# Optimization experiments

Measured on AMD Instinct MI355X. Metric: run time of the kernel, lower is better.

Reference implementation:

```python
import jax, jax.numpy as jnp
import numpy as np

B, T, C = 2, 1024, 2048
E, TOPK = 8, 2
F_MOE = 1408
F_SHARED = 5632


def setup_inputs() -> dict:
    key = jax.random.key(0)
    ks = jax.random.split(key, 9)
    s = 0.02
    return {
        "x": jax.random.normal(ks[0], (B, T, C), dtype=jnp.float32),
        "gate_w": jax.random.normal(ks[1], (E, C), dtype=jnp.float32) * s,
        "expert_fc1": jax.random.normal(ks[2], (E, F_MOE, C), dtype=jnp.float32) * s,
        "expert_fc2": jax.random.normal(ks[3], (E, F_MOE, C), dtype=jnp.float32) * s,
        "expert_proj": jax.random.normal(ks[4], (E, C, F_MOE), dtype=jnp.float32) * s,
        "shared_fc1": jax.random.normal(ks[5], (F_SHARED, C), dtype=jnp.float32) * s,
        "shared_fc2": jax.random.normal(ks[6], (F_SHARED, C), dtype=jnp.float32) * s,
        "shared_proj": jax.random.normal(ks[7], (C, F_SHARED), dtype=jnp.float32) * s,
        "shared_gate_w": jax.random.normal(ks[8], (1, C), dtype=jnp.float32) * s,
    }


def reference(x, gate_w, expert_fc1, expert_fc2, expert_proj,
              shared_fc1, shared_fc2, shared_proj, shared_gate_w):
    b, t, c = x.shape
    xf = x.reshape(-1, c)                                   # [N, C]
    n = xf.shape[0]

    # router: softmax in fp32, then top-k
    router = xf @ gate_w.T                                  # [N, E]
    probs = jax.nn.softmax(router.astype(jnp.float32), axis=1).astype(x.dtype)
    top_p, top_i = jax.lax.top_k(probs, TOPK)               # [N, k]

    # dense combine weights: prob where selected else 0 (top-k indices are distinct)
    combine = jnp.zeros((n, E), dtype=x.dtype).at[
        jnp.arange(n)[:, None], top_i].set(top_p)            # [N, E]

    # per-expert SwiGLU MLP, computed densely then weighted by combine
    h1 = jnp.einsum('nc,efc->enf', xf, expert_fc1)          # [E, N, F]
    h2 = jnp.einsum('nc,efc->enf', xf, expert_fc2)
    h = jax.nn.silu(h1) * h2
    out_e = jnp.einsum('enf,ecf->enc', h, expert_proj)      # [E, N, C]
    y = jnp.einsum('ne,enc->nc', combine, out_e)            # [N, C]

    # shared expert with sigmoid gate
    s1 = xf @ shared_fc1.T
    s2 = xf @ shared_fc2.T
    shared = (jax.nn.silu(s1) * s2) @ shared_proj.T         # [N, C]
    y = y + jax.nn.sigmoid(xf @ shared_gate_w.T) * shared
    return y.reshape(b, t, c)
```

## Files before the change

kernel.cpp:

```cpp
#include <hip/hip_runtime.h>
#include <hip/hip_bf16.h>
#include <math.h>
#include <stdint.h>

#define N_TOK   2048
#define C_DIM   2048
#define E_NUM   8
#define F_MOE   1408
#define F_SH    5632
#define SLOTS   4096
#define PADROWS 4608

typedef __bf16 bf16;
typedef __bf16 bf16x8 __attribute__((ext_vector_type(8)));
typedef __bf16 bf16x4 __attribute__((ext_vector_type(4)));
typedef float  f32x4  __attribute__((ext_vector_type(4)));

__device__ __forceinline__ f32x4 mfma16(bf16x8 a, bf16x8 b, f32x4 c) {
    return __builtin_amdgcn_mfma_f32_16x16x32_bf16(a, b, c, 0, 0, 0);
}
__device__ __forceinline__ void gload16(const void* g, void* l) {
    __builtin_amdgcn_global_load_lds(
        (const __attribute__((address_space(1))) void*)g,
        (__attribute__((address_space(3))) void*)l, 16, 0, 0);
}
#define RAWBAR()  asm volatile("s_barrier" ::: "memory")
#define VMCNT12() asm volatile("s_waitcnt vmcnt(12)" ::: "memory")
#define VMCNT8()  asm volatile("s_waitcnt vmcnt(8)" ::: "memory")
#define VMCNT4()  asm volatile("s_waitcnt vmcnt(4)" ::: "memory")
#define VMCNT0()  asm volatile("s_waitcnt vmcnt(0)" ::: "memory")

__global__ void router_kernel(const float* __restrict__ x,
                              const float* __restrict__ gate_w,
                              const float* __restrict__ sgate_w,
                              int* __restrict__ slotexp,
                              float* __restrict__ slotp,
                              float* __restrict__ sig)
{
    const int n   = blockIdx.x;
    const int tid = threadIdx.x;
    const float* xr = x + (size_t)n * C_DIM;
    const int c0 = tid * 8;

    float xv[8];
#pragma unroll
    for (int j = 0; j < 8; ++j) xv[j] = xr[c0 + j];

    float dots[9];
#pragma unroll
    for (int e = 0; e < 9; ++e) {
        const float* wr = (e < 8) ? (gate_w + (size_t)e * C_DIM) : sgate_w;
        float p = 0.f;
#pragma unroll
        for (int j = 0; j < 8; ++j) p += xv[j] * wr[c0 + j];
#pragma unroll
        for (int off = 32; off > 0; off >>= 1) p += __shfl_down(p, off);
        dots[e] = p;
    }

    __shared__ float red[4][9];
    const int wid = tid >> 6, lane = tid & 63;
    if (lane == 0) {
#pragma unroll
        for (int e = 0; e < 9; ++e) red[wid][e] = dots[e];
    }
    __syncthreads();
    if (tid == 0) {
        float l[9];
#pragma unroll
        for (int e = 0; e < 9; ++e)
            l[e] = red[0][e] + red[1][e] + red[2][e] + red[3][e];
        float mx = l[0];
#pragma unroll
        for (int e = 1; e < 8; ++e) mx = fmaxf(mx, l[e]);
        float p[8], s = 0.f;
#pragma unroll
        for (int e = 0; e < 8; ++e) { p[e] = expf(l[e] - mx); s += p[e]; }
        const float inv = 1.f / s;
#pragma unroll
        for (int e = 0; e < 8; ++e) p[e] *= inv;
        int i1 = 0;
#pragma unroll
        for (int e = 1; e < 8; ++e) if (p[e] > p[i1]) i1 = e;
        int i2 = (i1 == 0) ? 1 : 0;
#pragma unroll
        for (int e = 0; e < 8; ++e) if (e != i1 && p[e] > p[i2]) i2 = e;
        slotexp[2 * n]     = i1;  slotp[2 * n]     = p[i1];
        slotexp[2 * n + 1] = i2;  slotp[2 * n + 1] = p[i2];
        sig[n] = 1.f / (1.f + expf(-l[8]));
    }
}

__global__ void scatter_kernel(const int* __restrict__ slotexp,
                               int* __restrict__ counts, int* __restrict__ bases,
                               int* __restrict__ pos_of, int* __restrict__ row_token)
{
    const int tid = threadIdx.x;
    const int w = tid >> 6, lane = tid & 63;
    __shared__ int cnt[E_NUM], base[E_NUM];

    int run = 0;
    for (int s0 = 0; s0 < SLOTS; s0 += 64) {
        int e = slotexp[s0 + lane];
        unsigned long long m = __ballot(e == w);
        run += __popcll(m);
    }
    if (lane == 0) cnt[w] = run;
    __syncthreads();
    if (tid == 0) {
        int b = 0;
        for (int e = 0; e < E_NUM; ++e) { base[e] = b; b += cnt[e]; }
    }
    __syncthreads();
    run = 0;
    for (int s0 = 0; s0 < SLOTS; s0 += 64) {
        const int s = s0 + lane;
        const int e = slotexp[s];
        unsigned long long m = __ballot(e == w);
        if (e == w) {
            const unsigned long long lt = (lane == 0) ? 0ull : (~0ull >> (64 - lane));
            const int pos = base[w] + run + __popcll(m & lt);
            pos_of[s]      = pos;
            row_token[pos] = s >> 1;
        }
        run += __popcll(m);
    }
    if (lane == 0) { counts[w] = cnt[w]; bases[w] = base[w]; }
}

struct CvtArgs {
    const float* in[7];
    bf16*        out[7];
    int          cum[8];
};

__global__ void cvt_all_kernel(CvtArgs a)
{
    int b = blockIdx.x;
    int s = 0;
#pragma unroll
    for (int k = 1; k < 7; ++k) s += (b >= a.cum[k]);
    const size_t base = (size_t)(b - a.cum[s]) * 8192;
    const float* in = a.in[s];
    bf16* out = a.out[s];
    const int t4 = threadIdx.x * 4;
    f32x4 v[8];
#pragma unroll
    for (int c = 0; c < 8; ++c)
        v[c] = __builtin_nontemporal_load((const f32x4*)(in + base + c * 1024 + t4));
#pragma unroll
    for (int c = 0; c < 8; ++c) {
        bf16x4 o;
#pragma unroll
        for (int j = 0; j < 4; ++j) o[j] = (bf16)v[c][j];
        __builtin_nontemporal_store(o, (bf16x4*)(out + base + c * 1024 + t4));
    }
}

__global__ void gather_kernel(const bf16* __restrict__ Xs,
                              const int* __restrict__ row_token,
                              bf16* __restrict__ Xg)
{
    const int pos = blockIdx.x;
    const int t   = row_token[pos];
    const bf16x8* s = (const bf16x8*)(Xs + (size_t)t * C_DIM);
    bf16x8*       d = (bf16x8*)(Xg + (size_t)pos * C_DIM);
    d[threadIdx.x] = s[threadIdx.x];
}

template<bool DUAL, int KSPLIT>
__device__ __forceinline__ void gemm_body(
    const bf16* __restrict__ A, int lda,
    const bf16* __restrict__ B1g, const bf16* __restrict__ B2g, size_t strideB,
    bf16* __restrict__ OUTh, bf16* __restrict__ OUTq, int ldo, size_t strideOut,
    int base, int cnt, int e, int yt, int nt, int kp, int K, char* lds)
{
    const int KT = (K / 64) / KSPLIT;
    const int H  = 2 * KT;

    const int m0 = base + yt * 256;
    const int tid = threadIdx.x;
    const int w = tid >> 6, lane = tid & 63;

    const int l3  = lane >> 3;
    const int chS = (lane & 7) ^ l3;
    const int hiS = chS >> 2, ccS = chS & 3;
    const int rl  = w * 16 + 2 * l3 + hiS;
    const size_t lda2 = (size_t)lda * 2, K2 = (size_t)K * 2;
    const size_t kpoff = (size_t)kp * KT * 128;

    const char* aSrc0 = (const char*)A + (size_t)(m0 + rl)       * lda2 + ccS * 16 + kpoff;
    const char* aSrc1 = (const char*)A + (size_t)(m0 + 128 + rl) * lda2 + ccS * 16 + kpoff;
    const bf16* B1 = B1g + (size_t)e * strideB;
    const char* bSrc0;
    const char* bSrc1;
    if constexpr (DUAL) {
        const bf16* B2 = B2g + (size_t)e * strideB;
        bSrc0 = (const char*)B1 + (size_t)(nt * 128 + rl) * K2 + ccS * 16 + kpoff;
        bSrc1 = (const char*)B2 + (size_t)(nt * 128 + rl) * K2 + ccS * 16 + kpoff;
    } else {
        bSrc0 = (const char*)B1 + (size_t)(nt * 256 + rl)       * K2 + ccS * 16 + kpoff;
        bSrc1 = (const char*)B1 + (size_t)(nt * 256 + 128 + rl) * K2 + ccS * 16 + kpoff;
    }
    char* ldsw = lds + w * 1024;

    auto issue = [&](int h, int buf) {
        const size_t ko = (size_t)(h >> 1) * 128 + (size_t)(h & 1) * 64;
        char* d = ldsw + buf * 32768;
        gload16(aSrc0 + ko, d);
        gload16(aSrc1 + ko, d + 8192);
        gload16(bSrc0 + ko, d + 16384);
        gload16(bSrc1 + ko, d + 24576);
    };

    const int wm = w >> 2, wn = w & 3;
    const int fr = lane & 15, fq = lane >> 4;
    const int chRd = (((fr & 1) << 2) | fq) ^ ((fr >> 1) & 7);
    uint32_t aOff[8], bOff[4];
#pragma unroll
    for (int m = 0; m < 8; ++m)
        aOff[m] = (uint32_t)((wm * 64 + m * 8 + (fr >> 1)) * 128 + chRd * 16);
#pragma unroll
    for (int n = 0; n < 4; ++n) {
        int rp;
        if constexpr (DUAL)
            rp = (n < 2) ? (wn * 16 + n * 8) : (64 + wn * 16 + (n - 2) * 8);
        else
            rp = wn * 32 + n * 8;
        rp += (fr >> 1);
        bOff[n] = (uint32_t)(16384 + rp * 128 + chRd * 16);
    }

    f32x4 acc[8][4] = {};

    auto compute_half = [&](int buf) {
        const char* LB = lds + buf * 32768;
        bf16x8 af[4], ag[4], bf[4];
#pragma unroll
        for (int n = 0; n < 4; ++n) bf[n] = *(const bf16x8*)(LB + bOff[n]);
#pragma unroll
        for (int m = 0; m < 4; ++m) af[m] = *(const bf16x8*)(LB + aOff[m]);
#pragma unroll
        for (int m = 0; m < 4; ++m) ag[m] = *(const bf16x8*)(LB + aOff[4 + m]);
        __builtin_amdgcn_s_setprio(1);
#pragma unroll
        for (int m = 0; m < 4; ++m)
#pragma unroll
            for (int n = 0; n < 4; ++n)
                acc[m][n] = mfma16(af[m], bf[n], acc[m][n]);
#pragma unroll
        for (int m = 0; m < 4; ++m)
#pragma unroll
            for (int n = 0; n < 4; ++n)
                acc[4 + m][n] = mfma16(ag[m], bf[n], acc[4 + m][n]);
        __builtin_amdgcn_s_setprio(0);
    };

    issue(0, 0); issue(1, 1); issue(2, 2); issue(3, 3);

    int cur = 0, wr = 4;
    for (int h = 0; h < H - 4; ++h) {
        VMCNT12();
        RAWBAR();
        issue(h + 4, wr);
        compute_half(cur);
        cur = (cur == 4) ? 0 : cur + 1;
        wr  = (wr  == 4) ? 0 : wr  + 1;
    }
    VMCNT12(); RAWBAR(); compute_half(cur); cur = (cur == 4) ? 0 : cur + 1;
    VMCNT8();  RAWBAR(); compute_half(cur); cur = (cur == 4) ? 0 : cur + 1;
    VMCNT4();  RAWBAR(); compute_half(cur); cur = (cur == 4) ? 0 : cur + 1;
    VMCNT0();  RAWBAR(); compute_half(cur);

    const int rb0 = m0 + wm * 128;
    const int rend = base + cnt;
#pragma unroll
    for (int m = 0; m < 8; ++m) {
#pragma unroll
        for (int j = 0; j < 4; ++j) {
            const int grow = rb0 + m * 16 + fq * 4 + j;
            if (grow >= rend) continue;
            if constexpr (DUAL) {
#pragma unroll
                for (int n = 0; n < 2; ++n) {
                    const int gcol = nt * 128 + wn * 32 + n * 16 + fr;
                    const float h1 = acc[m][n][j];
                    const float h2 = acc[m][n + 2][j];
                    OUTh[(size_t)grow * ldo + gcol] =
                        (bf16)(h1 / (1.f + expf(-h1)) * h2);
                }
            } else {
                bf16* O = OUTq + (size_t)kp * strideOut;
#pragma unroll
                for (int n = 0; n < 4; ++n) {
                    const int gcol = nt * 256 + wn * 64 + n * 16 + fr;
                    O[(size_t)grow * ldo + gcol] = (bf16)acc[m][n][j];
                }
            }
        }
    }
}

template<bool DUAL, bool GROUPED, int KSPLIT>
__global__ __launch_bounds__(512, 1)
void gemm8(const bf16* __restrict__ A, int lda,
           const bf16* __restrict__ B1g, const bf16* __restrict__ B2g,
           size_t strideB,
           bf16* __restrict__ OUTh, bf16* __restrict__ OUTq, int ldo,
           size_t strideOut,
           const int* __restrict__ bases, const int* __restrict__ counts,
           int K)
{
    __shared__ char lds[163840];
    int e, yt, nt, kp, base, cnt;
    if constexpr (GROUPED) {
        e = blockIdx.x; yt = blockIdx.y; nt = blockIdx.z; kp = 0;
        base = bases[e]; cnt = counts[e];
        if (yt * 256 >= cnt) return;
    } else {
        nt = blockIdx.x; yt = blockIdx.y; kp = (KSPLIT > 1) ? blockIdx.z : 0;
        e = 0; base = 0; cnt = N_TOK;
    }
    gemm_body<DUAL, KSPLIT>(A, lda, B1g, B2g, strideB, OUTh, OUTq, ldo,
                            strideOut, base, cnt, e, yt, nt, kp, K, lds);
}

#define FC0_TILES 352

__global__ __launch_bounds__(512, 1)
void gemm_fc(const bf16* __restrict__ Xs, const bf16* __restrict__ Xg,
             const bf16* __restrict__ Wsfc1, const bf16* __restrict__ Wsfc2,
             const bf16* __restrict__ Wefc1, const bf16* __restrict__ Wefc2,
             bf16* __restrict__ Hs, bf16* __restrict__ Hm,
             const int* __restrict__ bases, const int* __restrict__ counts)
{
    __shared__ char lds[163840];
    const int id = blockIdx.x;
    if (id < FC0_TILES) {
        const int nt = id % 44, yt = id / 44;
        gemm_body<true, 1>(Xs, C_DIM, Wsfc1, Wsfc2, 0, Hs, nullptr, F_SH, 0,
                           0, N_TOK, 0, yt, nt, 0, C_DIM, lds);
    } else {
        const int lid = id - FC0_TILES;
        const int e = lid & 7, yt = (lid >> 3) & 15, nt = lid >> 7;
        const int base = bases[e], cnt = counts[e];
        if (yt * 256 >= cnt) return;
        gemm_body<true, 1>(Xg, C_DIM, Wefc1, Wefc2, (size_t)F_MOE * C_DIM,
                           Hm, nullptr, F_MOE, 0,
                           base, cnt, e, yt, nt, 0, C_DIM, lds);
    }
}

__global__ void combine_kernel(const bf16* __restrict__ SP,
                               const bf16* __restrict__ EP,
                               const int* __restrict__ pos_of,
                               const float* __restrict__ slotp,
                               const float* __restrict__ sig,
                               float* __restrict__ y)
{
    const int n  = blockIdx.x;
    const int p0 = pos_of[2 * n], p1 = pos_of[2 * n + 1];
    const float w0 = slotp[2 * n], w1 = slotp[2 * n + 1], sg = sig[n];
    const size_t PS = (size_t)N_TOK * C_DIM;
    const size_t cidx = (size_t)n * C_DIM + threadIdx.x * 8;

    bf16x8 s0 = *(const bf16x8*)(SP + cidx);
    bf16x8 s1 = *(const bf16x8*)(SP + cidx + PS);
    bf16x8 s2 = *(const bf16x8*)(SP + cidx + 2 * PS);
    bf16x8 s3 = *(const bf16x8*)(SP + cidx + 3 * PS);
    bf16x8 a0 = *(const bf16x8*)(EP + (size_t)p0 * C_DIM + threadIdx.x * 8);
    bf16x8 a1 = *(const bf16x8*)(EP + (size_t)p1 * C_DIM + threadIdx.x * 8);

    float out[8];
#pragma unroll
    for (int j = 0; j < 8; ++j) {
        const float ssum = (float)s0[j] + (float)s1[j] + (float)s2[j] + (float)s3[j];
        out[j] = sg * ssum + w0 * (float)a0[j] + w1 * (float)a1[j];
    }
    f32x4 o0, o1;
#pragma unroll
    for (int j = 0; j < 4; ++j) { o0[j] = out[j]; o1[j] = out[4 + j]; }
    *(f32x4*)(y + cidx)     = o0;
    *(f32x4*)(y + cidx + 4) = o1;
}

extern "C" void kernel_launch(void* const* d_in, const int* in_sizes, int n_in,
                              void* d_out, int out_size, void* d_ws, size_t ws_size,
                              hipStream_t stream)
{
    const float* x     = (const float*)d_in[0];
    const float* gatew = (const float*)d_in[1];
    const float* efc1  = (const float*)d_in[2];
    const float* efc2  = (const float*)d_in[3];
    const float* eproj = (const float*)d_in[4];
    const float* sfc1  = (const float*)d_in[5];
    const float* sfc2  = (const float*)d_in[6];
    const float* sproj = (const float*)d_in[7];
    const float* sgate = (const float*)d_in[8];
    float* y = (float*)d_out;

    char* w = (char*)d_ws;
    size_t off = 0;
    auto take = [&](size_t bytes) {
        char* p = w + off;
        off = (off + bytes + 255) & ~(size_t)255;
        return p;
    };
    int*   counts    = (int*)  take(E_NUM * 4);
    int*   bases     = (int*)  take(E_NUM * 4);
    int*   slotexp   = (int*)  take(SLOTS * 4);
    float* slotp     = (float*)take(SLOTS * 4);
    int*   pos_of    = (int*)  take(SLOTS * 4);
    int*   row_token = (int*)  take(PADROWS * 4);
    float* sig       = (float*)take(N_TOK * 4);
    bf16*  Xs        = (bf16*) take((size_t)N_TOK   * C_DIM * 2);
    bf16*  Xg        = (bf16*) take((size_t)PADROWS * C_DIM * 2);
    bf16*  Hs        = (bf16*) take((size_t)N_TOK   * F_SH  * 2);
    bf16*  Hm        = (bf16*) take((size_t)PADROWS * F_MOE * 2);
    bf16*  SP        = (bf16*) take((size_t)4 * N_TOK * C_DIM * 2);
    bf16*  EP        = (bf16*) take((size_t)PADROWS * C_DIM * 2);
    bf16*  Wefc1     = (bf16*) take((size_t)E_NUM * F_MOE * C_DIM * 2);
    bf16*  Wefc2     = (bf16*) take((size_t)E_NUM * F_MOE * C_DIM * 2);
    bf16*  Weproj    = (bf16*) take((size_t)E_NUM * C_DIM * F_MOE * 2);
    bf16*  Wsfc1     = (bf16*) take((size_t)F_SH * C_DIM * 2);
    bf16*  Wsfc2     = (bf16*) take((size_t)F_SH * C_DIM * 2);
    bf16*  Wsproj    = (bf16*) take((size_t)C_DIM * F_SH * 2);
    (void)ws_size; (void)in_sizes; (void)n_in; (void)out_size;

    CvtArgs ca;
    const int nbx  = (N_TOK * C_DIM) / 8192;
    const int nbe  = (E_NUM * F_MOE * C_DIM) / 8192;
    const int nbs  = (F_SH * C_DIM) / 8192;
    ca.in[0] = x;     ca.out[0] = Xs;
    ca.in[1] = efc1;  ca.out[1] = Wefc1;
    ca.in[2] = efc2;  ca.out[2] = Wefc2;
    ca.in[3] = eproj; ca.out[3] = Weproj;
    ca.in[4] = sfc1;  ca.out[4] = Wsfc1;
    ca.in[5] = sfc2;  ca.out[5] = Wsfc2;
    ca.in[6] = sproj; ca.out[6] = Wsproj;
    ca.cum[0] = 0;
    ca.cum[1] = nbx;
    ca.cum[2] = nbx + nbe;
    ca.cum[3] = nbx + 2 * nbe;
    ca.cum[4] = nbx + 3 * nbe;
    ca.cum[5] = nbx + 3 * nbe + nbs;
    ca.cum[6] = nbx + 3 * nbe + 2 * nbs;
    ca.cum[7] = nbx + 3 * nbe + 3 * nbs;
    cvt_all_kernel<<<ca.cum[7], 256, 0, stream>>>(ca);

    router_kernel<<<N_TOK, 256, 0, stream>>>(x, gatew, sgate, slotexp, slotp, sig);
    scatter_kernel<<<1, 512, 0, stream>>>(slotexp, counts, bases, pos_of, row_token);
    gather_kernel<<<SLOTS, 256, 0, stream>>>(Xs, row_token, Xg);

    gemm_fc<<<FC0_TILES + E_NUM * (SLOTS / 256) * (F_MOE / 128), 512, 0, stream>>>(
        Xs, Xg, Wsfc1, Wsfc2, Wefc1, Wefc2, Hs, Hm, bases, counts);

    gemm8<false, false, 4><<<dim3(C_DIM / 256, N_TOK / 256, 4), 512, 0, stream>>>(
        Hs, F_SH, Wsproj, nullptr, 0, nullptr, SP, C_DIM, (size_t)N_TOK * C_DIM,
        nullptr, nullptr, F_SH);

    gemm8<false, true, 1><<<dim3(E_NUM, SLOTS / 256, C_DIM / 256), 512, 0, stream>>>(
        Hm, F_MOE, Weproj, nullptr, (size_t)C_DIM * F_MOE, nullptr, EP, C_DIM, 0,
        bases, counts, F_MOE);

    combine_kernel<<<N_TOK, 256, 0, stream>>>(SP, EP, pos_of, slotp, sig, y);
}
```

Before: 429.7 us.

## Double-buffer LDS fragment registers to overlap LDS reads with MFMA

Restructures the GEMM main loop into a register-level software pipeline. Each step now reads the next stage's A/B fragments from LDS into a second register set before issuing the MFMAs on the current set, and the loop is unrolled by two with an explicit epilogue. The goal is to hide LDS read latency behind matrix-core work. In exchange it doubles fragment register usage, which may reduce occupancy or cause spills. It also changes the vmcnt waits and the order in which LDS buffers are recycled, and assumes H-4 is even.

```diff
diff --git a/kernel.cpp b/kernel.cpp
--- a/kernel.cpp
+++ b/kernel.cpp
@@ -233,44 +233,50 @@
 
     f32x4 acc[8][4] = {};
 
-    auto compute_half = [&](int buf) {
+    bf16x8 A0[8], B0[4], A1[8], B1f[4];
+
+    auto readfrags = [&](int buf, bf16x8 (&FA)[8], bf16x8 (&FB)[4]) {
         const char* LB = lds + buf * 32768;
-        bf16x8 af[4], ag[4], bf[4];
-#pragma unroll
-        for (int n = 0; n < 4; ++n) bf[n] = *(const bf16x8*)(LB + bOff[n]);
-#pragma unroll
-        for (int m = 0; m < 4; ++m) af[m] = *(const bf16x8*)(LB + aOff[m]);
-#pragma unroll
-        for (int m = 0; m < 4; ++m) ag[m] = *(const bf16x8*)(LB + aOff[4 + m]);
+#pragma unroll
+        for (int n = 0; n < 4; ++n) FB[n] = *(const bf16x8*)(LB + bOff[n]);
+#pragma unroll
+        for (int m = 0; m < 8; ++m) FA[m] = *(const bf16x8*)(LB + aOff[m]);
+    };
+    auto mfmahalf = [&](bf16x8 (&FA)[8], bf16x8 (&FB)[4]) {
         __builtin_amdgcn_s_setprio(1);
 #pragma unroll
-        for (int m = 0; m < 4; ++m)
+        for (int m = 0; m < 8; ++m)
 #pragma unroll
             for (int n = 0; n < 4; ++n)
-                acc[m][n] = mfma16(af[m], bf[n], acc[m][n]);
-#pragma unroll
-        for (int m = 0; m < 4; ++m)
-#pragma unroll
-            for (int n = 0; n < 4; ++n)
-                acc[4 + m][n] = mfma16(ag[m], bf[n], acc[4 + m][n]);
+                acc[m][n] = mfma16(FA[m], FB[n], acc[m][n]);
         __builtin_amdgcn_s_setprio(0);
     };
 
     issue(0, 0); issue(1, 1); issue(2, 2); issue(3, 3);
-
-    int cur = 0, wr = 4;
-    for (int h = 0; h < H - 4; ++h) {
-        VMCNT12();
-        RAWBAR();
-        issue(h + 4, wr);
-        compute_half(cur);
-        cur = (cur == 4) ? 0 : cur + 1;
-        wr  = (wr  == 4) ? 0 : wr  + 1;
-    }
-    VMCNT12(); RAWBAR(); compute_half(cur); cur = (cur == 4) ? 0 : cur + 1;
-    VMCNT8();  RAWBAR(); compute_half(cur); cur = (cur == 4) ? 0 : cur + 1;
-    VMCNT4();  RAWBAR(); compute_half(cur); cur = (cur == 4) ? 0 : cur + 1;
-    VMCNT0();  RAWBAR(); compute_half(cur);
+    VMCNT12(); RAWBAR();
+    readfrags(0, A0, B0);
+
+    int rdbuf = 1, wrbuf = 4;
+    for (int it = 0; it < (H - 4) / 2; ++it) {
+        VMCNT8(); RAWBAR();
+        readfrags(rdbuf, A1, B1f); rdbuf = (rdbuf == 4) ? 0 : rdbuf + 1;
+        issue(2 * it + 4, wrbuf);  wrbuf = (wrbuf == 4) ? 0 : wrbuf + 1;
+        mfmahalf(A0, B0);
+        VMCNT8(); RAWBAR();
+        readfrags(rdbuf, A0, B0); rdbuf = (rdbuf == 4) ? 0 : rdbuf + 1;
+        issue(2 * it + 5, wrbuf); wrbuf = (wrbuf == 4) ? 0 : wrbuf + 1;
+        mfmahalf(A1, B1f);
+    }
+    VMCNT8(); RAWBAR();
+    readfrags(rdbuf, A1, B1f); rdbuf = (rdbuf == 4) ? 0 : rdbuf + 1;
+    mfmahalf(A0, B0);
+    VMCNT4(); RAWBAR();
+    readfrags(rdbuf, A0, B0); rdbuf = (rdbuf == 4) ? 0 : rdbuf + 1;
+    mfmahalf(A1, B1f);
+    VMCNT0(); RAWBAR();
+    readfrags(rdbuf, A1, B1f);
+    mfmahalf(A0, B0);
+    mfmahalf(A1, B1f);
 
     const int rb0 = m0 + wm * 128;
     const int rend = base + cnt;
```

Result: no change. 435.5 us (+1.3%).

## Move projection weight conversion into the fc GEMM launch as trailing blocks

Applied to the files above, without the earlier changes.

Expert and shared projection weights are now converted from fp32 to bf16 by extra blocks appended to the fused fc GEMM grid, instead of in the up-front conversion kernel. The intent is to hide this memory-bound conversion behind or alongside the compute-bound fc GEMM tiles and shorten the serial conversion phase. The risk is that the conversion blocks are scheduled after all GEMM tiles under a one-block-per-CU launch bound, giving a long tail with little real overlap, and they also compete for bandwidth.

```diff
diff --git a/kernel.cpp b/kernel.cpp
--- a/kernel.cpp
+++ b/kernel.cpp
@@ -129,9 +129,9 @@
 }
 
 struct CvtArgs {
-    const float* in[7];
-    bf16*        out[7];
-    int          cum[8];
+    const float* in[5];
+    bf16*        out[5];
+    int          cum[6];
 };
 
 __global__ void cvt_all_kernel(CvtArgs a)
@@ -139,7 +139,7 @@
     int b = blockIdx.x;
     int s = 0;
 #pragma unroll
-    for (int k = 1; k < 7; ++k) s += (b >= a.cum[k]);
+    for (int k = 1; k < 5; ++k) s += (b >= a.cum[k]);
     const size_t base = (size_t)(b - a.cum[s]) * 8192;
     const float* in = a.in[s];
     bf16* out = a.out[s];
@@ -326,12 +326,17 @@
 }
 
 #define FC0_TILES 352
+#define FC_TILES  1760
+#define CVT_EP_BLKS 1408
+#define CVT_SP_BLKS 704
 
 __global__ __launch_bounds__(512, 1)
 void gemm_fc(const bf16* __restrict__ Xs, const bf16* __restrict__ Xg,
              const bf16* __restrict__ Wsfc1, const bf16* __restrict__ Wsfc2,
              const bf16* __restrict__ Wefc1, const bf16* __restrict__ Wefc2,
              bf16* __restrict__ Hs, bf16* __restrict__ Hm,
+             const float* __restrict__ eproj, const float* __restrict__ sproj,
+             bf16* __restrict__ Weproj, bf16* __restrict__ Wsproj,
              const int* __restrict__ bases, const int* __restrict__ counts)
 {
     __shared__ char lds[163840];
@@ -340,7 +345,7 @@
         const int nt = id % 44, yt = id / 44;
         gemm_body<true, 1>(Xs, C_DIM, Wsfc1, Wsfc2, 0, Hs, nullptr, F_SH, 0,
                            0, N_TOK, 0, yt, nt, 0, C_DIM, lds);
-    } else {
+    } else if (id < FC_TILES) {
         const int lid = id - FC0_TILES;
         const int e = lid & 7, yt = (lid >> 3) & 15, nt = lid >> 7;
         const int base = bases[e], cnt = counts[e];
@@ -348,6 +353,25 @@
         gemm_body<true, 1>(Xg, C_DIM, Wefc1, Wefc2, (size_t)F_MOE * C_DIM,
                            Hm, nullptr, F_MOE, 0,
                            base, cnt, e, yt, nt, 0, C_DIM, lds);
+    } else {
+        const int cid = id - FC_TILES;
+        const float* in;
+        bf16* out;
+        size_t base;
+        if (cid < CVT_EP_BLKS) { in = eproj; out = Weproj; base = (size_t)cid * 16384; }
+        else { in = sproj; out = Wsproj; base = (size_t)(cid - CVT_EP_BLKS) * 16384; }
+        const int t4 = threadIdx.x * 4;
+        f32x4 v[8];
+#pragma unroll
+        for (int c = 0; c < 8; ++c)
+            v[c] = __builtin_nontemporal_load((const f32x4*)(in + base + c * 2048 + t4));
+#pragma unroll
+        for (int c = 0; c < 8; ++c) {
+            bf16x4 o;
+#pragma unroll
+            for (int j = 0; j < 4; ++j) o[j] = (bf16)v[c][j];
+            __builtin_nontemporal_store(o, (bf16x4*)(out + base + c * 2048 + t4));
+        }
     }
 }
 
@@ -434,26 +458,23 @@
     ca.in[0] = x;     ca.out[0] = Xs;
     ca.in[1] = efc1;  ca.out[1] = Wefc1;
     ca.in[2] = efc2;  ca.out[2] = Wefc2;
-    ca.in[3] = eproj; ca.out[3] = Weproj;
-    ca.in[4] = sfc1;  ca.out[4] = Wsfc1;
-    ca.in[5] = sfc2;  ca.out[5] = Wsfc2;
-    ca.in[6] = sproj; ca.out[6] = Wsproj;
+    ca.in[3] = sfc1;  ca.out[3] = Wsfc1;
+    ca.in[4] = sfc2;  ca.out[4] = Wsfc2;
     ca.cum[0] = 0;
     ca.cum[1] = nbx;
     ca.cum[2] = nbx + nbe;
     ca.cum[3] = nbx + 2 * nbe;
-    ca.cum[4] = nbx + 3 * nbe;
-    ca.cum[5] = nbx + 3 * nbe + nbs;
-    ca.cum[6] = nbx + 3 * nbe + 2 * nbs;
-    ca.cum[7] = nbx + 3 * nbe + 3 * nbs;
-    cvt_all_kernel<<<ca.cum[7], 256, 0, stream>>>(ca);
+    ca.cum[4] = nbx + 2 * nbe + nbs;
+    ca.cum[5] = nbx + 2 * nbe + 2 * nbs;
+    cvt_all_kernel<<<ca.cum[5], 256, 0, stream>>>(ca);
 
     router_kernel<<<N_TOK, 256, 0, stream>>>(x, gatew, sgate, slotexp, slotp, sig);
     scatter_kernel<<<1, 512, 0, stream>>>(slotexp, counts, bases, pos_of, row_token);
     gather_kernel<<<SLOTS, 256, 0, stream>>>(Xs, row_token, Xg);
 
-    gemm_fc<<<FC0_TILES + E_NUM * (SLOTS / 256) * (F_MOE / 128), 512, 0, stream>>>(
-        Xs, Xg, Wsfc1, Wsfc2, Wefc1, Wefc2, Hs, Hm, bases, counts);
+    gemm_fc<<<FC_TILES + CVT_EP_BLKS + CVT_SP_BLKS, 512, 0, stream>>>(
+        Xs, Xg, Wsfc1, Wsfc2, Wefc1, Wefc2, Hs, Hm,
+        eproj, sproj, Weproj, Wsproj, bases, counts);
 
     gemm8<false, false, 4><<<dim3(C_DIM / 256, N_TOK / 256, 4), 512, 0, stream>>>(
         Hs, F_SH, Wsproj, nullptr, 0, nullptr, SP, C_DIM, (size_t)N_TOK * C_DIM,
```

Result: faster. 408.6 us (-4.9%).
